# Kernel optimization log

Hardware: AMD Instinct MI355X
Metric: run time of the kernel (lower is better)

Reference implementation:

```python
import jax, jax.numpy as jnp
import numpy as np

EPS = 1e-5
GROUPS = 4
KSZ = 3
PAD = 1
CUTON = 0.1


def conv1x1(x, w):
    # x: [b,c,h,w], w: [o,c,1,1]
    return jnp.einsum('bchw,oc->bohw', x, w[:, :, 0, 0])


def bn_eval(x, g, b, m, v):
    scale = g / jnp.sqrt(v + EPS)
    return (x - m[None, :, None, None]) * scale[None, :, None, None] + b[None, :, None, None]


def extract_patches(xp, k):
    # xp: [b,c,H+2p,W+2p] -> [b,c,h,w,k,k] (matches torch unfold(2,k,1).unfold(3,k,1))
    h = xp.shape[2] - k + 1
    w = xp.shape[3] - k + 1
    p = jnp.stack([xp[:, :, i:i + h, j:j + w] for i in range(k) for j in range(k)], axis=-1)
    return p.reshape(p.shape[:-1] + (k, k))


def batch_fftshift(z):
    # faithful to roll_n with n = d//2 (+1 if odd), over dims 1..3; roll_n == roll by -n
    for ax in (1, 2, 3):
        d = z.shape[ax]
        z = jnp.roll(z, -(d // 2 + (d % 2)), axis=ax)
    return z


def batch_ifftshift(z):
    for ax in (3, 2, 1):
        z = jnp.roll(z, -(z.shape[ax] // 2), axis=ax)
    return z


def attention_conv(x, yq, q_w, k_w, v_w, rel_h, rel_w):
    b, c, h, w = x.shape
    C = q_w.shape[0]
    px = jnp.pad(x, ((0, 0), (0, 0), (PAD, PAD), (PAD, PAD)))
    q = conv1x1(yq, q_w)                      # [b,C,h,w]
    k = conv1x1(px, k_w)
    v = conv1x1(px, v_w)
    kp = extract_patches(k, KSZ)              # [b,C,h,w,3,3]
    vp = extract_patches(v, KSZ)
    kh, kw = kp[:, :C // 2], kp[:, C // 2:]
    kp = jnp.concatenate([kh + rel_h, kw + rel_w], axis=1)
    kp = kp.reshape(b, GROUPS, C // GROUPS, h, w, KSZ * KSZ)
    vp = vp.reshape(b, GROUPS, C // GROUPS, h, w, KSZ * KSZ)
    q = q.reshape(b, GROUPS, C // GROUPS, h, w, 1)
    attn = jax.nn.softmax(q * kp, axis=-1)
    out = jnp.einsum('bgchwk,bgchwk->bgchw', attn, vp)
    return out.reshape(b, C, h, w)


def fam(x, rate1, rate2, w1, w0_w, w0_b):
    h, w = x.shape[2], x.shape[3]
    # torch.fft.fftn with dim=None -> FFT over ALL dims (batch & channel too)
    x_ft = jnp.fft.fftn(x, norm='ortho')
    out_ft = jnp.einsum('bixy,ioxy->boxy', x_ft, w1)
    s = batch_fftshift(out_ft)
    cy, cx = h // 2, w // 2
    rh, rw = int(CUTON * cy), int(CUTON * cx)
    mask = jnp.ones((h, w), dtype=x.dtype).at[cy - rh:cy + rh, cx - rw:cx + rw].set(0.0)
    s = s * mask
    out_ft = batch_ifftshift(s)
    # torch.fft.ifftn with s=(h,w) -> inverse FFT over last two dims only
    out = jnp.fft.ifftn(out_ft, s=(h, w), norm='ortho').real
    out2 = conv1x1(x, w0_w) + w0_b[None, :, None, None]
    return rate1 * out + rate2 * out2


def setup_inputs() -> dict:
    key = jax.random.key(0)
    ks = jax.random.split(key, 16)
    B, Cx, Cy, M, O, H, W = 4, 128, 256, 128, 128, 64, 64
    scale = 1.0 / (M * O)
    inp = {
        'x': jax.random.normal(ks[0], (B, Cx, H, W), jnp.float32),
        'y': jax.random.normal(ks[1], (B, Cy, H // 2, W // 2), jnp.float32),
        'conv1_w': jax.random.normal(ks[2], (M, Cy, 1, 1), jnp.float32) * 0.05,
        'bn1_g': jnp.ones((M,), jnp.float32),
        'bn1_b': jnp.zeros((M,), jnp.float32),
        'bn1_m': jnp.zeros((M,), jnp.float32),
        'bn1_v': jnp.ones((M,), jnp.float32),
        'q_w': jax.random.normal(ks[3], (M, M, 1, 1), jnp.float32) * 0.05,
        'k_w': jax.random.normal(ks[4], (M, M, 1, 1), jnp.float32) * 0.05,
        'v_w': jax.random.normal(ks[5], (M, M, 1, 1), jnp.float32) * 0.05,
        'rel_h': jax.random.normal(ks[6], (M // 2, 1, 1, 3, 1), jnp.float32),
        'rel_w': jax.random.normal(ks[7], (M // 2, 1, 1, 1, 3), jnp.float32),
        'rate1': jnp.full((1,), 0.5, jnp.float32),
        'rate2': jnp.full((1,), 0.5, jnp.float32),
        'w1_real': scale * jax.random.uniform(ks[8], (M, O, H, W), jnp.float32),
        'w1_imag': scale * jax.random.uniform(ks[9], (M, O, H, W), jnp.float32),
        'w0_w': jax.random.normal(ks[10], (O, M, 1, 1), jnp.float32) * 0.05,
        'w0_b': jnp.zeros((O,), jnp.float32),
        'bn2_g': jnp.ones((O,), jnp.float32),
        'bn2_b': jnp.zeros((O,), jnp.float32),
        'bn2_m': jnp.zeros((O,), jnp.float32),
        'bn2_v': jnp.ones((O,), jnp.float32),
    }
    return inp


def reference(x, y, conv1_w, bn1_g, bn1_b, bn1_m, bn1_v, q_w, k_w, v_w, rel_h, rel_w,
              rate1, rate2, w1_real, w1_imag, w0_w, w0_b, bn2_g, bn2_b, bn2_m, bn2_v):
    # conv1 (teacher proj) + BN + ReLU
    y1 = jax.nn.relu(bn_eval(conv1x1(y, conv1_w), bn1_g, bn1_b, bn1_m, bn1_v))
    # nearest interpolate to x spatial size (torch 'nearest': idx = floor(i*in/out))
    H, W = x.shape[2], x.shape[3]
    ih = (jnp.arange(H) * y1.shape[2]) // H
    iw = (jnp.arange(W) * y1.shape[3]) // W
    y_up = y1[:, :, ih][:, :, :, iw]
    # local unfold attention
    x_att = attention_conv(x, y_up, q_w, k_w, v_w, rel_h, rel_w)
    # FAM spectral branch + BN + ReLU
    w1 = jax.lax.complex(w1_real, w1_imag)
    y_out = jax.nn.relu(bn_eval(fam(x_att, rate1, rate2, w1, w0_w, w0_b),
                                bn2_g, bn2_b, bn2_m, bn2_v))
    return (y_out, x_att)
```

## Files before the change

kernel.cpp:

```cpp
#include <hip/hip_runtime.h>

#define BB 4
#define CY 256
#define CM 128
#define HW 4096
#define HWy 1024
#define PHW 4356
#define EPSF 1e-5f
#define TWOPI 6.2831853071795864769f

struct c32 { float re, im; };


__global__ void conv1_kernel(const float* __restrict__ y, const float* __restrict__ w,
                             const float* __restrict__ g, const float* __restrict__ bb,
                             const float* __restrict__ m, const float* __restrict__ v,
                             float* __restrict__ y1){
  int p = blockIdx.x*256 + threadIdx.x;
  int ocb = blockIdx.y*8;
  int b = blockIdx.z;
  float acc[8] = {0,0,0,0,0,0,0,0};
  const float* yb = y + (size_t)b*CY*HWy + p;
  #pragma unroll 4
  for(int ic=0; ic<CY; ic++){
    float xv = yb[(size_t)ic*HWy];
    #pragma unroll
    for(int j=0;j<8;j++) acc[j] += xv * w[(ocb+j)*CY + ic];
  }
  #pragma unroll
  for(int j=0;j<8;j++){
    int oc = ocb+j;
    float s = g[oc]*rsqrtf(v[oc]+EPSF);
    float bi = bb[oc] - m[oc]*s;
    float r = acc[j]*s + bi;
    y1[((size_t)(b*CM+oc))*HWy + p] = r>0.f?r:0.f;
  }
}

__global__ void qconv_kernel(const float* __restrict__ y1, const float* __restrict__ w,
                             float* __restrict__ q){
  int p = blockIdx.x*256 + threadIdx.x;
  int ocb = blockIdx.y*8; int b = blockIdx.z;
  int mi = ((p>>7)<<5) + ((p&63)>>1);
  float acc[8] = {0,0,0,0,0,0,0,0};
  const float* yb = y1 + (size_t)b*CM*HWy + mi;
  #pragma unroll 4
  for(int ic=0; ic<CM; ic++){
    float xv = yb[(size_t)ic*HWy];
    #pragma unroll
    for(int j=0;j<8;j++) acc[j] += xv * w[(ocb+j)*CM+ic];
  }
  #pragma unroll
  for(int j=0;j<8;j++) q[((size_t)(b*CM+ocb+j))*HW + p] = acc[j];
}

__global__ void kvconv_kernel(const float* __restrict__ x, const float* __restrict__ kw,
                              const float* __restrict__ vw,
                              float* __restrict__ k, float* __restrict__ v){
  int p = blockIdx.x*256 + threadIdx.x;
  int ocb = blockIdx.y*8; int b = blockIdx.z;
  if(p >= PHW) return;
  int hh = p/66, ww2 = p - hh*66;
  int ih = hh-1, iw = ww2-1;
  bool inb = (ih>=0 && ih<64 && iw>=0 && iw<64);
  float acck[8] = {0,0,0,0,0,0,0,0};
  float accv[8] = {0,0,0,0,0,0,0,0};
  if(inb){
    const float* xb = x + (size_t)b*CM*HW + ih*64 + iw;
    #pragma unroll 4
    for(int ic=0; ic<CM; ic++){
      float xv = xb[(size_t)ic*HW];
      #pragma unroll
      for(int j=0;j<8;j++){ acck[j] += xv*kw[(ocb+j)*CM+ic]; accv[j] += xv*vw[(ocb+j)*CM+ic]; }
    }
  }
  #pragma unroll
  for(int j=0;j<8;j++){
    size_t o = ((size_t)(b*CM+ocb+j))*PHW + p;
    k[o]=acck[j]; v[o]=accv[j];
  }
}


__global__ void attn_kernel(const float* __restrict__ q, const float* __restrict__ k,
                            const float* __restrict__ v, const float* __restrict__ relh,
                            const float* __restrict__ relw, float* __restrict__ xatt){
  int t = blockIdx.x*256 + threadIdx.x;
  int p = t & 4095;
  int bc = t >> 12;
  int c = bc & 127;
  int h = p>>6, w2 = p&63;
  float qv = q[(size_t)bc*HW + p];
  const float* kb = k + (size_t)bc*PHW;
  const float* vb = v + (size_t)bc*PHW;
  float lg[9], vv[9];
  #pragma unroll
  for(int ti=0; ti<3; ti++){
    #pragma unroll
    for(int tj=0; tj<3; tj++){
      int idx = (h+ti)*66 + (w2+tj);
      float rel = (c<64) ? relh[c*3+ti] : relw[(c-64)*3+tj];
      float kv = kb[idx] + rel;
      lg[ti*3+tj] = qv*kv;
      vv[ti*3+tj] = vb[idx];
    }
  }
  float mx = lg[0];
  #pragma unroll
  for(int i=1;i<9;i++) mx = fmaxf(mx, lg[i]);
  float s=0.f, o=0.f;
  #pragma unroll
  for(int i=0;i<9;i++){ float e = __expf(lg[i]-mx); s += e; o += e*vv[i]; }
  xatt[t] = o/s;
}


template<int SIGN>
__device__ inline void dft8(const c32* a, c32* X){
  constexpr float C8[8] = {1.f,0.70710678118654752f,0.f,-0.70710678118654752f,
                           -1.f,-0.70710678118654752f,0.f,0.70710678118654752f};
  constexpr float S8[8] = {0.f,0.70710678118654752f,1.f,0.70710678118654752f,
                           0.f,-0.70710678118654752f,-1.f,-0.70710678118654752f};
  #pragma unroll
  for(int kk=0;kk<8;kk++){
    float xr=0.f, xi=0.f;
    #pragma unroll
    for(int n=0;n<8;n++){
      const int j=(n*kk)&7;
      const float wr = C8[j];
      const float wi = SIGN*S8[j];
      xr += a[n].re*wr - a[n].im*wi;
      xi += a[n].re*wi + a[n].im*wr;
    }
    X[kk].re=xr; X[kk].im=xi;
  }
}

template<int SIGN, bool RIN, bool ROUT>
__global__ void fft64_kernel(const float* in, float* out,
                             int l_div, int s1, int s2, int estride, float scale){
  __shared__ c32 tmp[32][65];
  int ll = threadIdx.x & 31;
  int j  = threadIdx.x >> 5;
  int l = blockIdx.x*32 + ll;
  int base = (l/l_div)*s1 + (l%l_div)*s2;
  c32 a[8];
  #pragma unroll
  for(int n1=0;n1<8;n1++){
    int e = n1*8 + j;
    if(RIN){ a[n1].re = in[base + e*estride]; a[n1].im = 0.f; }
    else { const float2* ci = (const float2*)in; float2 t2 = ci[base + e*estride]; a[n1].re=t2.x; a[n1].im=t2.y; }
  }
  c32 A[8];
  dft8<SIGN>(a, A);
  #pragma unroll
  for(int k1=0;k1<8;k1++){
    float ang = SIGN * (TWOPI/64.f) * (float)(j*k1);
    float sn, cs; __sincosf(ang, &sn, &cs);
    c32 t; t.re = A[k1].re*cs - A[k1].im*sn; t.im = A[k1].re*sn + A[k1].im*cs;
    tmp[ll][k1*8+j] = t;
  }
  __syncthreads();
  c32 bv[8];
  #pragma unroll
  for(int n2=0;n2<8;n2++) bv[n2] = tmp[ll][j*8+n2];
  c32 Y[8];
  dft8<SIGN>(bv, Y);
  #pragma unroll
  for(int k2=0;k2<8;k2++){
    int e = j + 8*k2;
    int oi = base + e*estride;
    if(ROUT) out[oi] = Y[k2].re*scale;
    else { float2* co = (float2*)out; co[oi] = make_float2(Y[k2].re*scale, Y[k2].im*scale); }
  }
}

template<int SIGN>
__global__ void fft128_kernel(float* data, float scale){
  __shared__ c32 tmp[16][129];
  int ll = threadIdx.x & 15;
  int j  = threadIdx.x >> 4;
  int l = blockIdx.x*16 + ll;
  int b = l >> 12;
  int rem = l & 4095;
  size_t base = (size_t)b*CM*HW + rem;
  float2* cd = (float2*)data;
  c32 a[8];
  #pragma unroll
  for(int n1=0;n1<8;n1++){
    float2 t2 = cd[base + (size_t)(16*n1 + j)*HW];
    a[n1].re=t2.x; a[n1].im=t2.y;
  }
  c32 A[8];
  dft8<SIGN>(a, A);
  #pragma unroll
  for(int k1=0;k1<8;k1++){
    float ang = SIGN*(TWOPI/128.f)*(float)(j*k1);
    float sn,cs; __sincosf(ang,&sn,&cs);
    c32 t; t.re = A[k1].re*cs - A[k1].im*sn; t.im = A[k1].re*sn + A[k1].im*cs;
    tmp[ll][k1*16 + j] = t;
  }
  __syncthreads();
  int k1 = j & 7, half = j >> 3;
  c32 bv[16];
  #pragma unroll
  for(int n2=0;n2<16;n2++) bv[n2] = tmp[ll][k1*16+n2];
  #pragma unroll
  for(int kk=0;kk<8;kk++){
    int k2 = half*8 + kk;
    float xr=0.f, xi=0.f;
    #pragma unroll
    for(int n2=0;n2<16;n2++){
      float ang = SIGN*(TWOPI/16.f)*(float)((n2*k2)&15);
      float sn,cs; __sincosf(ang,&sn,&cs);
      xr += bv[n2].re*cs - bv[n2].im*sn;
      xi += bv[n2].re*sn + bv[n2].im*cs;
    }
    cd[base + (size_t)(k1 + 8*k2)*HW] = make_float2(xr*scale, xi*scale);
  }
}

__global__ void einsum_kernel(const float2* __restrict__ Xf, const float* __restrict__ w1r,
                              const float* __restrict__ w1i, float2* __restrict__ OutF){
  int L = blockIdx.x;
  int wk = (L & 7) * 256 + (L >> 3);
  int obase = (wk & 31) * 4;
  int fbase = (wk >> 5) * 64;
  int fl = threadIdx.x & 63;
  int ol = threadIdx.x >> 6;
  int f = fbase + fl;
  int o = obase + ol;
  c32 acc[4];
  #pragma unroll
  for(int kb=0;kb<4;kb++){ acc[kb].re=0.f; acc[kb].im=0.f; }
  const float2* X0 = Xf + f;
  const float* wr_base = w1r + (size_t)o*HW + f;
  const float* wi_base = w1i + (size_t)o*HW + f;
  for(int i=0;i<CM;i++){
    float2 x0 = X0[(size_t)(0*CM + i)*HW];
    float2 x1 = X0[(size_t)(1*CM + i)*HW];
    float2 x2 = X0[(size_t)(2*CM + i)*HW];
    float2 x3 = X0[(size_t)(3*CM + i)*HW];
    c32 Xb[4];
    Xb[0].re = x0.x+x1.x+x2.x+x3.x;      Xb[0].im = x0.y+x1.y+x2.y+x3.y;
    Xb[1].re = x0.x + x1.y - x2.x - x3.y; Xb[1].im = x0.y - x1.x - x2.y + x3.x;
    Xb[2].re = x0.x - x1.x + x2.x - x3.x; Xb[2].im = x0.y - x1.y + x2.y - x3.y;
    Xb[3].re = x0.x - x1.y - x2.x + x3.y; Xb[3].im = x0.y + x1.x - x2.y - x3.x;
    size_t wo = (size_t)i*CM*HW;
    float wr  = wr_base[wo];
    float wim = wi_base[wo];
    #pragma unroll
    for(int kb=0;kb<4;kb++){
      acc[kb].re += Xb[kb].re*wr - Xb[kb].im*wim;
      acc[kb].im += Xb[kb].re*wim + Xb[kb].im*wr;
    }
  }
  int hf = f>>6, wf = f&63;
  bool masked = (hf<3 || hf>60) && (wf<3 || wf>60);
  #pragma unroll
  for(int kb=0;kb<4;kb++){
    float2 t2 = masked ? make_float2(0.f,0.f) : make_float2(acc[kb].re, acc[kb].im);
    OutF[((size_t)(kb*CM + o))*HW + f] = t2;
  }
}

__global__ void final_kernel(const float* __restrict__ G, const float* __restrict__ xatt,
                             const float* __restrict__ w0, const float* __restrict__ w0b,
                             const float* __restrict__ r1p, const float* __restrict__ r2p,
                             const float* __restrict__ g2, const float* __restrict__ b2,
                             const float* __restrict__ m2, const float* __restrict__ v2,
                             float* __restrict__ yout){
  int p = blockIdx.x*256 + threadIdx.x;
  int ocb = blockIdx.y*8; int b = blockIdx.z;
  float r1 = r1p[0], r2 = r2p[0];
  float acc[8] = {0,0,0,0,0,0,0,0};
  const float* xb = xatt + (size_t)b*CM*HW + p;
  #pragma unroll 4
  for(int ic=0; ic<CM; ic++){
    float xv = xb[(size_t)ic*HW];
    #pragma unroll
    for(int j=0;j<8;j++) acc[j] += xv * w0[(ocb+j)*CM + ic];
  }
  #pragma unroll
  for(int j=0;j<8;j++){
    int oc = ocb+j;
    float fam = r1 * G[((size_t)(b*CM+oc))*HW + p] + r2*(acc[j] + w0b[oc]);
    float s = g2[oc]*rsqrtf(v2[oc]+EPSF);
    float bi = b2[oc] - m2[oc]*s;
    float val = fam*s + bi;
    yout[((size_t)(b*CM+oc))*HW + p] = val>0.f?val:0.f;
  }
}

extern "C" void kernel_launch(void* const* d_in, const int* in_sizes, int n_in,
                              void* d_out, int out_size, void* d_ws, size_t ws_size,
                              hipStream_t stream){
  const float* x       = (const float*)d_in[0];
  const float* y       = (const float*)d_in[1];
  const float* conv1_w = (const float*)d_in[2];
  const float* bn1_g   = (const float*)d_in[3];
  const float* bn1_b   = (const float*)d_in[4];
  const float* bn1_m   = (const float*)d_in[5];
  const float* bn1_v   = (const float*)d_in[6];
  const float* q_w     = (const float*)d_in[7];
  const float* k_w     = (const float*)d_in[8];
  const float* v_w     = (const float*)d_in[9];
  const float* rel_h   = (const float*)d_in[10];
  const float* rel_w   = (const float*)d_in[11];
  const float* rate1   = (const float*)d_in[12];
  const float* rate2   = (const float*)d_in[13];
  const float* w1r     = (const float*)d_in[14];
  const float* w1i     = (const float*)d_in[15];
  const float* w0_w    = (const float*)d_in[16];
  const float* w0_b    = (const float*)d_in[17];
  const float* bn2_g   = (const float*)d_in[18];
  const float* bn2_b   = (const float*)d_in[19];
  const float* bn2_m   = (const float*)d_in[20];
  const float* bn2_v   = (const float*)d_in[21];
  (void)in_sizes; (void)n_in; (void)out_size; (void)ws_size;

  char* ws = (char*)d_ws;
  float* Y1 = (float*)(ws + 0);
  float* Q  = (float*)(ws + 2097152);
  float* K  = (float*)(ws + 10485760);
  float* V  = (float*)(ws + 19406848);
  float2* E = (float2*)(ws + 0);
  float2* F = (float2*)(ws + 16777216);
  float*  G = (float*)(ws + 0);

  float* yout = (float*)d_out;
  float* xatt = (float*)d_out + 2097152;

  conv1_kernel<<<dim3(4,16,BB),256,0,stream>>>(y, conv1_w, bn1_g,bn1_b,bn1_m,bn1_v, Y1);
  qconv_kernel<<<dim3(16,16,BB),256,0,stream>>>(Y1, q_w, Q);
  kvconv_kernel<<<dim3(18,16,BB),256,0,stream>>>(x, k_w, v_w, K, V);
  attn_kernel<<<dim3(8192),256,0,stream>>>(Q, K, V, rel_h, rel_w, xatt);

  fft64_kernel<-1,true,false><<<dim3(1024),256,0,stream>>>(xatt, (float*)E, 64,4096,64, 1, 0.125f);
  fft64_kernel<-1,false,false><<<dim3(1024),256,0,stream>>>((float*)E, (float*)E, 64,4096,1, 64, 0.125f);
  fft128_kernel<-1><<<dim3(1024),256,0,stream>>>((float*)E, 0.044194173824159216f);
  einsum_kernel<<<dim3(2048),256,0,stream>>>(E, w1r, w1i, F);
  fft64_kernel<1,false,false><<<dim3(1024),256,0,stream>>>((float*)F, (float*)F, 64,4096,1, 64, 0.125f);
  fft64_kernel<1,false,true><<<dim3(1024),256,0,stream>>>((float*)F, G, 64,4096,64, 1, 0.125f);

  final_kernel<<<dim3(16,16,BB),256,0,stream>>>(G, xatt, w0_w, w0_b, rate1, rate2,
                                                bn2_g,bn2_b,bn2_m,bn2_v, yout);
}
```

Before: 816.5 us.

## Precompute batch-dim DFT in separate kernel and vectorize spectral einsum loads

Moves the size-4 DFT across the batch dimension out of the einsum into a standalone kernel so it runs once rather than per output-channel group. The einsum now processes two frequencies per thread using float4 activation loads and float2 weight loads, with launch bounds and a halved grid. Workspace buffers are remapped to avoid aliasing. This adds an extra pass over the spectrum in exchange for wider, less redundant loads in the bandwidth-heavy einsum.

```diff
diff --git a/kernel.cpp b/kernel.cpp
--- a/kernel.cpp
+++ b/kernel.cpp
@@ -220,48 +220,78 @@
   }
 }
 
-__global__ void einsum_kernel(const float2* __restrict__ Xf, const float* __restrict__ w1r,
-                              const float* __restrict__ w1i, float2* __restrict__ OutF){
+__global__ void fft4b_kernel(const float4* __restrict__ E4, float4* __restrict__ Eb4){
+  int t = blockIdx.x*256 + threadIdx.x;
+  int i  = t >> 11;
+  int fp = t & 2047;
+  float4 x0 = E4[(size_t)(0*CM+i)*2048 + fp];
+  float4 x1 = E4[(size_t)(1*CM+i)*2048 + fp];
+  float4 x2 = E4[(size_t)(2*CM+i)*2048 + fp];
+  float4 x3 = E4[(size_t)(3*CM+i)*2048 + fp];
+  float4 y0, y1, y2, y3;
+  y0.x = x0.x+x1.x+x2.x+x3.x;       y0.y = x0.y+x1.y+x2.y+x3.y;
+  y1.x = x0.x + x1.y - x2.x - x3.y; y1.y = x0.y - x1.x - x2.y + x3.x;
+  y2.x = x0.x - x1.x + x2.x - x3.x; y2.y = x0.y - x1.y + x2.y - x3.y;
+  y3.x = x0.x - x1.y - x2.x + x3.y; y3.y = x0.y + x1.x - x2.y - x3.x;
+  y0.z = x0.z+x1.z+x2.z+x3.z;       y0.w = x0.w+x1.w+x2.w+x3.w;
+  y1.z = x0.z + x1.w - x2.z - x3.w; y1.w = x0.w - x1.z - x2.w + x3.z;
+  y2.z = x0.z - x1.z + x2.z - x3.z; y2.w = x0.w - x1.w + x2.w - x3.w;
+  y3.z = x0.z - x1.w - x2.z + x3.w; y3.w = x0.w + x1.z - x2.w - x3.z;
+  Eb4[(size_t)(0*CM+i)*2048 + fp] = y0;
+  Eb4[(size_t)(1*CM+i)*2048 + fp] = y1;
+  Eb4[(size_t)(2*CM+i)*2048 + fp] = y2;
+  Eb4[(size_t)(3*CM+i)*2048 + fp] = y3;
+}
+
+#define CMAC(A, B, W_r, W_i) \
+  A.x += B.x*W_r.x - B.y*W_i.x; \
+  A.y += B.x*W_i.x + B.y*W_r.x; \
+  A.z += B.z*W_r.y - B.w*W_i.y; \
+  A.w += B.z*W_i.y + B.w*W_r.y;
+
+__global__ __launch_bounds__(256,4)
+void einsum_kernel(const float4* __restrict__ Xb4, const float2* __restrict__ w1r2,
+                   const float2* __restrict__ w1i2, float4* __restrict__ OutF4){
   int L = blockIdx.x;
-  int wk = (L & 7) * 256 + (L >> 3);
+  int wk = (L & 7) * 128 + (L >> 3);
   int obase = (wk & 31) * 4;
-  int fbase = (wk >> 5) * 64;
+  int fbase = (wk >> 5) * 128;
   int fl = threadIdx.x & 63;
   int ol = threadIdx.x >> 6;
-  int f = fbase + fl;
-  int o = obase + ol;
-  c32 acc[4];
-  #pragma unroll
-  for(int kb=0;kb<4;kb++){ acc[kb].re=0.f; acc[kb].im=0.f; }
-  const float2* X0 = Xf + f;
-  const float* wr_base = w1r + (size_t)o*HW + f;
-  const float* wi_base = w1i + (size_t)o*HW + f;
+  int f0 = fbase + fl*2;
+  int o  = obase + ol;
+  int fp = f0 >> 1;
+  float4 acc0 = make_float4(0.f,0.f,0.f,0.f);
+  float4 acc1 = make_float4(0.f,0.f,0.f,0.f);
+  float4 acc2 = make_float4(0.f,0.f,0.f,0.f);
+  float4 acc3 = make_float4(0.f,0.f,0.f,0.f);
+  const float4* X0 = Xb4 + fp;
+  const float2* wr0 = w1r2 + (size_t)o*2048 + fp;
+  const float2* wi0 = w1i2 + (size_t)o*2048 + fp;
+  #pragma unroll 4
   for(int i=0;i<CM;i++){
-    float2 x0 = X0[(size_t)(0*CM + i)*HW];
-    float2 x1 = X0[(size_t)(1*CM + i)*HW];
-    float2 x2 = X0[(size_t)(2*CM + i)*HW];
-    float2 x3 = X0[(size_t)(3*CM + i)*HW];
-    c32 Xb[4];
-    Xb[0].re = x0.x+x1.x+x2.x+x3.x;      Xb[0].im = x0.y+x1.y+x2.y+x3.y;
-    Xb[1].re = x0.x + x1.y - x2.x - x3.y; Xb[1].im = x0.y - x1.x - x2.y + x3.x;
-    Xb[2].re = x0.x - x1.x + x2.x - x3.x; Xb[2].im = x0.y - x1.y + x2.y - x3.y;
-    Xb[3].re = x0.x - x1.y - x2.x + x3.y; Xb[3].im = x0.y + x1.x - x2.y - x3.x;
-    size_t wo = (size_t)i*CM*HW;
-    float wr  = wr_base[wo];
-    float wim = wi_base[wo];
-    #pragma unroll
-    for(int kb=0;kb<4;kb++){
-      acc[kb].re += Xb[kb].re*wr - Xb[kb].im*wim;
-      acc[kb].im += Xb[kb].re*wim + Xb[kb].im*wr;
-    }
-  }
-  int hf = f>>6, wf = f&63;
-  bool masked = (hf<3 || hf>60) && (wf<3 || wf>60);
-  #pragma unroll
-  for(int kb=0;kb<4;kb++){
-    float2 t2 = masked ? make_float2(0.f,0.f) : make_float2(acc[kb].re, acc[kb].im);
-    OutF[((size_t)(kb*CM + o))*HW + f] = t2;
-  }
+    float4 b0 = X0[(size_t)(0*CM+i)*2048];
+    float4 b1 = X0[(size_t)(1*CM+i)*2048];
+    float4 b2 = X0[(size_t)(2*CM+i)*2048];
+    float4 b3 = X0[(size_t)(3*CM+i)*2048];
+    float2 wr = wr0[(size_t)i*CM*2048];
+    float2 wi = wi0[(size_t)i*CM*2048];
+    CMAC(acc0, b0, wr, wi)
+    CMAC(acc1, b1, wr, wi)
+    CMAC(acc2, b2, wr, wi)
+    CMAC(acc3, b3, wr, wi)
+  }
+  int hf = f0>>6;
+  int wf0 = f0&63, wf1 = wf0+1;
+  bool mh = (hf<3 || hf>60);
+  bool m0 = mh && (wf0<3 || wf0>60);
+  bool m1 = mh && (wf1<3 || wf1>60);
+  if(m0){ acc0.x=0.f;acc0.y=0.f; acc1.x=0.f;acc1.y=0.f; acc2.x=0.f;acc2.y=0.f; acc3.x=0.f;acc3.y=0.f; }
+  if(m1){ acc0.z=0.f;acc0.w=0.f; acc1.z=0.f;acc1.w=0.f; acc2.z=0.f;acc2.w=0.f; acc3.z=0.f;acc3.w=0.f; }
+  OutF4[((size_t)(0*CM + o))*2048 + fp] = acc0;
+  OutF4[((size_t)(1*CM + o))*2048 + fp] = acc1;
+  OutF4[((size_t)(2*CM + o))*2048 + fp] = acc2;
+  OutF4[((size_t)(3*CM + o))*2048 + fp] = acc3;
 }
 
 __global__ void final_kernel(const float* __restrict__ G, const float* __restrict__ xatt,
@@ -324,9 +354,10 @@
   float* Q  = (float*)(ws + 2097152);
   float* K  = (float*)(ws + 10485760);
   float* V  = (float*)(ws + 19406848);
-  float2* E = (float2*)(ws + 0);
-  float2* F = (float2*)(ws + 16777216);
-  float*  G = (float*)(ws + 0);
+  float2* E  = (float2*)(ws + 0);
+  float2* Eb = (float2*)(ws + 16777216);
+  float2* F  = (float2*)(ws + 0);
+  float*  G  = (float*)(ws + 16777216);
 
   float* yout = (float*)d_out;
   float* xatt = (float*)d_out + 2097152;
@@ -339,7 +370,9 @@
   fft64_kernel<-1,true,false><<<dim3(1024),256,0,stream>>>(xatt, (float*)E, 64,4096,64, 1, 0.125f);
   fft64_kernel<-1,false,false><<<dim3(1024),256,0,stream>>>((float*)E, (float*)E, 64,4096,1, 64, 0.125f);
   fft128_kernel<-1><<<dim3(1024),256,0,stream>>>((float*)E, 0.044194173824159216f);
-  einsum_kernel<<<dim3(2048),256,0,stream>>>(E, w1r, w1i, F);
+  fft4b_kernel<<<dim3(1024),256,0,stream>>>((const float4*)E, (float4*)Eb);
+  einsum_kernel<<<dim3(1024),256,0,stream>>>((const float4*)Eb, (const float2*)w1r,
+                                             (const float2*)w1i, (float4*)F);
   fft64_kernel<1,false,false><<<dim3(1024),256,0,stream>>>((float*)F, (float*)F, 64,4096,1, 64, 0.125f);
   fft64_kernel<1,false,true><<<dim3(1024),256,0,stream>>>((float*)F, G, 64,4096,64, 1, 0.125f);
 
```

Result: slower. 1.104 ms (+35.2%).
